# Kernel tuning notes

Measured on AMD Instinct MI355X. Metric: run time of the kernel, lower is better.

Reference implementation:

```python
import jax, jax.numpy as jnp
import numpy as np

H = 128        # hidden_dim
R = 50         # num_rbf
L = 4          # num_layers
CUTOFF = 5.0
N = 10000      # atoms
M = 64         # molecules
BOX = 54.7     # box side -> ~32 neighbors within cutoff
EPS = 1e-5     # LayerNorm eps (torch default)


def setup_inputs() -> dict:
    rng = np.random.default_rng(0)
    positions = rng.uniform(0.0, BOX, size=(N, 3)).astype(np.float32)
    # static radius graph (the torch module filters a dense NxN pair list by cutoff;
    # we do that once here so runtime shapes are fixed / jit-friendly)
    sq = (positions ** 2).sum(-1)
    d2 = sq[:, None] + sq[None, :] - 2.0 * positions @ positions.T
    mask = (d2 < CUTOFF * CUTOFF) & ~np.eye(N, dtype=bool)
    row, col = np.nonzero(mask)
    edge_index = jnp.asarray(np.stack([row, col]).astype(np.int32))  # [2, E]

    key = jax.random.key(0)
    ks = jax.random.split(key, 6)
    s = 0.05
    return dict(
        atomic_numbers=jax.random.randint(ks[0], (N,), 0, 100),
        positions=jnp.asarray(positions),
        batch=jnp.asarray((np.arange(N) * M // N).astype(np.int32)),  # sorted, all M present
        edge_index=edge_index,
        embedding=jax.random.normal(ks[1], (100, H), jnp.float32) * s,
        W1=jax.random.normal(ks[2], (L, H + R, H), jnp.float32) * s,
        b1=jnp.zeros((L, H), jnp.float32),
        W2=jax.random.normal(ks[3], (L, H, H), jnp.float32) * s,
        b2=jnp.zeros((L, H), jnp.float32),
        W_ih=jax.random.normal(ks[4], (L, H, 3 * H), jnp.float32) * s,
        b_ih=jax.random.normal(ks[5], (L, 3 * H), jnp.float32) * s,
        b_hh=jnp.zeros((L, 3 * H), jnp.float32),
        ln_g=jnp.ones((H,), jnp.float32),
        ln_b=jnp.zeros((H,), jnp.float32),
    )


def reference(atomic_numbers, positions, batch, edge_index, embedding,
              W1, b1, W2, b2, W_ih, b_ih, b_hh, ln_g, ln_b):
    x = embedding[jnp.clip(atomic_numbers, 0, 99)]                  # [N, H]
    row, col = edge_index[0], edge_index[1]
    d = jnp.linalg.norm(positions[row] - positions[col], axis=-1)   # [E]
    centers = jnp.linspace(0.0, CUTOFF, R)
    width = CUTOFF / R
    rbf = jnp.exp(-((d[:, None] - centers) ** 2) / (2.0 * width * width))  # [E, R]
    n_atoms = x.shape[0]
    for l in range(L):
        x_j = x[row]                                                # gather [E, H]
        inp = jnp.concatenate([x_j, rbf], axis=-1)                  # [E, H+R]
        msg = jax.nn.silu(inp @ W1[l] + b1[l]) @ W2[l] + b2[l]      # [E, H]
        aggr = jax.ops.segment_sum(msg, col, num_segments=n_atoms)  # [N, H]
        # GRU step with h0 = 0: W_hh @ h vanishes, only b_hh survives
        gi = aggr @ W_ih[l] + b_ih[l]                               # [N, 3H]
        gi_r, gi_z, gi_n = jnp.split(gi, 3, axis=-1)
        bh_r, bh_z, bh_n = jnp.split(b_hh[l], 3)
        r = jax.nn.sigmoid(gi_r + bh_r)
        z = jax.nn.sigmoid(gi_z + bh_z)
        n = jnp.tanh(gi_n + r * bh_n)
        x = x + (1.0 - z) * n                                       # h' = (1-z)*n + z*0
    mu = x.mean(-1, keepdims=True)
    var = ((x - mu) ** 2).mean(-1, keepdims=True)
    x = (x - mu) / jnp.sqrt(var + EPS) * ln_g + ln_b
    sums = jax.ops.segment_sum(x, batch, num_segments=M)            # [M, H]
    counts = jax.ops.segment_sum(jnp.ones((x.shape[0],), jnp.float32), batch, num_segments=M)
    graph_rep = sums / jnp.clip(counts, 1.0)[:, None]
    return x, graph_rep
```

## Files before the change

kernel.cpp:

```cpp
#include <hip/hip_runtime.h>
#include <hip/hip_bf16.h>
#include <math.h>


#define HH 128
#define RR 50
#define LL 4
#define L2E 1.4426950408889634f

typedef __attribute__((ext_vector_type(8))) short short8;
typedef __attribute__((ext_vector_type(4))) float floatx4;

__device__ __forceinline__ unsigned short f2bf(float f) {
    unsigned u = __float_as_uint(f);
    unsigned r = (u + 0x7fffu + ((u >> 16) & 1u)) >> 16;
    return (unsigned short)r;
}
__device__ __forceinline__ unsigned pack_bf2(float lo, float hi) {
    unsigned u0 = __float_as_uint(lo) + 0x8000u;
    unsigned u1 = __float_as_uint(hi) + 0x8000u;
    return __builtin_amdgcn_perm(u1, u0, 0x07060302);
}
__device__ __forceinline__ float fast_sigmoid(float x) {
    return __builtin_amdgcn_rcpf(1.f + __builtin_amdgcn_exp2f(x * (-L2E)));
}
__device__ __forceinline__ float fast_tanh(float x) {
    x = fminf(fmaxf(x, -15.f), 15.f);
    float t = __builtin_amdgcn_exp2f(x * (2.f * L2E));
    return (t - 1.f) * __builtin_amdgcn_rcpf(t + 1.f);
}
__device__ __forceinline__ int imin(int a, int b) { return a < b ? a : b; }

__global__ __launch_bounds__(256) void prep_kernel(
    const int* __restrict__ an, const float* __restrict__ emb,
    float* __restrict__ X,
    const float* __restrict__ pos, const int* __restrict__ erow,
    const int* __restrict__ ecol, float* __restrict__ dist,
    int* __restrict__ rowptr, int* __restrict__ bptr,
    const int* __restrict__ batch,
    const float* __restrict__ W1, unsigned short* __restrict__ W1rT,
    unsigned short* __restrict__ W1xT,
    const float* __restrict__ W2, const float* __restrict__ Wih,
    unsigned short* __restrict__ WcT,
    const float* __restrict__ b2, float* __restrict__ P,
    int N, int E, int M)
{
    int gidx = blockIdx.x * 256 + threadIdx.x;
    int c0 = N * HH;
    if (gidx < c0) {
        int i = gidx >> 7, n = gidx & 127;
        int z = an[i];
        z = z < 0 ? 0 : (z > 99 ? 99 : z);
        X[gidx] = emb[z * HH + n];
        return;
    }
    gidx -= c0;
    int PT = E > N ? E : N;
    if (gidx < PT) {
        int i = gidx;
        if (i < E) {
            int rc = erow[i];
            int rp = (i > 0) ? erow[i - 1] : -1;
            for (int r = rp + 1; r <= rc; ++r) rowptr[r] = i;
            if (i == E - 1)
                for (int r = rc + 1; r <= N; ++r) rowptr[r] = E;
        }
        if (i < N) {
            int bc = batch[i];
            int bp = (i > 0) ? batch[i - 1] : -1;
            for (int m = bp + 1; m <= bc; ++m) bptr[m] = i;
            if (i == N - 1)
                for (int m = bc + 1; m <= M; ++m) bptr[m] = N;
        }
        return;
    }
    gidx -= PT;
    if (gidx < E) {
        int e = gidx;
        int r = erow[e], c = ecol[e];
        float dx = pos[r * 3 + 0] - pos[c * 3 + 0];
        float dy = pos[r * 3 + 1] - pos[c * 3 + 1];
        float dz = pos[r * 3 + 2] - pos[c * 3 + 2];
        dist[e] = sqrtf(dx * dx + dy * dy + dz * dz);
        return;
    }
    gidx -= E;
    if (gidx < LL * HH * 64) {
        int l = gidx >> 13, rem = gidx & 8191;
        int f = rem >> 9, lane2 = (rem >> 3) & 63, j = rem & 7;
        int nt = f >> 1, h = f & 1;
        int n = nt * 16 + (lane2 & 15);
        int k = h * 32 + (lane2 >> 4) * 8 + j;
        float v = (k < RR) ? W1[((size_t)l * 178 + 128 + k) * HH + n] : 0.f;
        W1rT[gidx] = f2bf(v);
        return;
    }
    gidx -= LL * HH * 64;
    if (gidx < LL * HH * HH) {
        int l = gidx >> 14, rem = gidx & 16383, n = rem >> 7, k = rem & 127;
        W1xT[gidx] = f2bf(W1[((size_t)l * 178 + k) * HH + n]);
        return;
    }
    gidx -= LL * HH * HH;
    if (gidx < LL * HH * 384) {
        int l = gidx / (HH * 384), rem = gidx % (HH * 384);
        int i = rem / 384, j = rem % 384;
        const float* w2row = W2 + ((size_t)l * HH + i) * HH;
        const float* wih = Wih + (size_t)l * HH * 384;
        float acc = 0.f;
#pragma unroll 4
        for (int k = 0; k < HH; ++k)
            acc = fmaf(w2row[k], wih[(size_t)k * 384 + j], acc);
        WcT[((size_t)l * 384 + j) * HH + i] = f2bf(acc);
        return;
    }
    gidx -= LL * HH * 384;
    if (gidx < LL * 384) {
        int l = gidx / 384, j = gidx % 384;
        const float* b2l = b2 + (size_t)l * HH;
        const float* wih = Wih + (size_t)l * HH * 384;
        float acc = 0.f;
#pragma unroll 4
        for (int k = 0; k < HH; ++k)
            acc = fmaf(b2l[k], wih[(size_t)k * 384 + j], acc);
        P[gidx] = acc;
    }
}

#define XAB 32
__global__ __launch_bounds__(256) void xw_kernel(
    const float* __restrict__ X, const float* __restrict__ W,
    const float* __restrict__ bias, unsigned short* __restrict__ XWb, int N)
{
    __shared__ __align__(16) float A[XAB][HH];
    int tid = threadIdx.x;
    int abase = blockIdx.x * XAB;
    for (int idx = tid; idx < XAB * HH; idx += 256) {
        int a = idx >> 7, k = idx & 127;
        A[a][k] = (abase + a < N) ? X[(size_t)(abase + a) * HH + k] : 0.f;
    }
    __syncthreads();
    int n = tid & 127, s = tid >> 7;
    float acc[16];
#pragma unroll
    for (int i = 0; i < 16; ++i) acc[i] = 0.f;
    for (int kc = 0; kc < 32; ++kc) {
        float w0 = W[(4 * kc + 0) * HH + n];
        float w1 = W[(4 * kc + 1) * HH + n];
        float w2 = W[(4 * kc + 2) * HH + n];
        float w3 = W[(4 * kc + 3) * HH + n];
#pragma unroll
        for (int i = 0; i < 16; ++i) {
            float4 av = *(const float4*)&A[s * 16 + i][4 * kc];
            acc[i] = fmaf(av.x, w0, acc[i]);
            acc[i] = fmaf(av.y, w1, acc[i]);
            acc[i] = fmaf(av.z, w2, acc[i]);
            acc[i] = fmaf(av.w, w3, acc[i]);
        }
    }
    float b = bias[n];
#pragma unroll
    for (int i = 0; i < 16; ++i) {
        int a = abase + s * 16 + i;
        if (a < N) XWb[(size_t)a * HH + n] = f2bf(acc[i] + b);
    }
}

__global__ __launch_bounds__(256) void edge_mfma_kernel(
    const unsigned short* __restrict__ XWb, const unsigned short* __restrict__ W1rTf,
    const float* __restrict__ dist, const int* __restrict__ rowptr,
    const int* __restrict__ ecol, unsigned short* __restrict__ Sbf,
    int N, int nwaves)
{
    __shared__ __align__(16) unsigned short W1s[8192];
    int tid = threadIdx.x;
    {
        const uint4* src = (const uint4*)W1rTf;
        uint4* dst = (uint4*)W1s;
#pragma unroll
        for (int i = 0; i < 4; ++i) dst[tid + i * 256] = src[tid + i * 256];
    }
    __syncthreads();

    int wid = (blockIdx.x << 2) + (tid >> 6);
    int lane = tid & 63;
    int c = lane & 15, q = lane >> 4;

    const float stepc = 5.0f / 49.0f;
    const float negc = -50.f * L2E;
    float kqs = (float)(q << 3) * stepc;

    int NW = 2 * N;
    for (int w = wid; w < NW; w += nwaves) {
        int a = w >> 1, h = w & 1;
        int es = rowptr[a], ee = rowptr[a + 1];
        float acc[4][4];
#pragma unroll
        for (int t = 0; t < 4; ++t)
#pragma unroll
            for (int r = 0; r < 4; ++r) acc[t][r] = 0.f;

        if (es < ee) {
            int last = ee - 1;
            int ce0 = imin(es + c, last);
            float dcur = dist[ce0];
            int colcur = ecol[ce0];
            int ce1 = imin(es + 16 + c, last);
            float dnxt = dist[ce1];
            int colnxt = ecol[ce1];

            for (int eb = es; eb < ee; eb += 16) {
                const unsigned short* xwrow = XWb + (size_t)colcur * HH + h * 64;
                uint2 gx[4];
#pragma unroll
                for (int t = 0; t < 4; ++t)
                    gx[t] = *(const uint2*)&xwrow[t * 16 + (q << 2)];

                float d_t = dcur;
                dcur = dnxt; colcur = colnxt;
                int ce2 = imin(eb + 32 + c, last);
                dnxt = dist[ce2];
                colnxt = ecol[ce2];

                float dq0 = d_t - kqs;
                float dq1 = dq0 - 32.f * stepc;
                union { unsigned u[4]; short8 s; } ub0, ub1;
#pragma unroll
                for (int p = 0; p < 4; ++p) {
                    float t0 = dq0 - (float)(2 * p) * stepc;
                    float t1 = dq0 - (float)(2 * p + 1) * stepc;
                    float e0f = __builtin_amdgcn_exp2f(negc * t0 * t0);
                    float e1f = __builtin_amdgcn_exp2f(negc * t1 * t1);
                    ub0.u[p] = pack_bf2(e0f, e1f);
                    float t2 = dq1 - (float)(2 * p) * stepc;
                    float t3 = dq1 - (float)(2 * p + 1) * stepc;
                    float e2f = __builtin_amdgcn_exp2f(negc * t2 * t2);
                    float e3f = __builtin_amdgcn_exp2f(negc * t3 * t3);
                    ub1.u[p] = pack_bf2(e2f, e3f);
                }
                short8 B0 = ub0.s, B1 = ub1.s;
                float msk = ((eb + c) < ee) ? 1.f : 0.f;

                unsigned wbyte = (unsigned)(lane * 16);
                asm volatile("" : "+v"(wbyte));
                const char* Wlp = (const char*)W1s + wbyte;

#pragma unroll
                for (int t = 0; t < 4; ++t) {
                    int f0 = (h * 4 + t) * 2;
                    short8 A0 = *(const short8*)(Wlp + f0 * 1024);
                    short8 A1 = *(const short8*)(Wlp + (f0 + 1) * 1024);
                    floatx4 C;
                    C[0] = __uint_as_float(gx[t].x << 16);
                    C[1] = __uint_as_float(gx[t].x & 0xffff0000u);
                    C[2] = __uint_as_float(gx[t].y << 16);
                    C[3] = __uint_as_float(gx[t].y & 0xffff0000u);
                    C = __builtin_amdgcn_mfma_f32_16x16x32_bf16(A0, B0, C, 0, 0, 0);
                    C = __builtin_amdgcn_mfma_f32_16x16x32_bf16(A1, B1, C, 0, 0, 0);
#pragma unroll
                    for (int r = 0; r < 4; ++r) {
                        float hh = C[r];
                        float v = hh * fast_sigmoid(hh);
                        acc[t][r] = fmaf(v, msk, acc[t][r]);
                    }
                }
            }
        }

        int b0 = c & 1, b1 = (c >> 1) & 1, b2 = (c >> 2) & 1, b3 = (c >> 3) & 1;
        float s1[4][2];
#pragma unroll
        for (int t = 0; t < 4; ++t)
#pragma unroll
            for (int p = 0; p < 2; ++p) {
                float keep = b0 ? acc[t][2 * p + 1] : acc[t][2 * p];
                float send = b0 ? acc[t][2 * p] : acc[t][2 * p + 1];
                s1[t][p] = keep + __shfl_xor(send, 1, 64);
            }
        float s2[4];
#pragma unroll
        for (int t = 0; t < 4; ++t) {
            float keep = b1 ? s1[t][1] : s1[t][0];
            float send = b1 ? s1[t][0] : s1[t][1];
            s2[t] = keep + __shfl_xor(send, 2, 64);
        }
        float s3[2];
#pragma unroll
        for (int u = 0; u < 2; ++u) {
            float keep = b2 ? s2[2 * u + 1] : s2[2 * u];
            float send = b2 ? s2[2 * u] : s2[2 * u + 1];
            s3[u] = keep + __shfl_xor(send, 4, 64);
        }
        float keep = b3 ? s3[1] : s3[0];
        float send = b3 ? s3[0] : s3[1];
        float fin = keep + __shfl_xor(send, 8, 64);

        int t_fin = 2 * b3 + b2;
        int r_fin = 2 * b1 + b0;
        int n = t_fin * 16 + (q << 2) + r_fin;
        Sbf[(size_t)a * HH + h * 64 + n] = f2bf(fin);
    }
}

#define GA 32
__global__ __launch_bounds__(256) void grux_mfma_kernel(
    const unsigned short* __restrict__ Sbf, const unsigned short* __restrict__ WcT,
    const float* __restrict__ P, const float* __restrict__ bih,
    const float* __restrict__ bhh, const int* __restrict__ rowptr,
    float* __restrict__ X, int N,
    const unsigned short* __restrict__ W1xT, const float* __restrict__ b1next,
    unsigned short* __restrict__ XWb, int do_xw)
{
    __shared__ __align__(16) unsigned short Sb[GA][136];
    __shared__ __align__(16) unsigned short Xb[GA][136];
    int tid = threadIdx.x;
    int abase = blockIdx.x * GA;
    int w = tid >> 6, lane = tid & 63, c = lane & 15, q = lane >> 4;

    float pn[2][3], bi[2][3], bh[2][3], deg[2][4];
#pragma unroll
    for (int t = 0; t < 2; ++t) {
        int n = w * 32 + t * 16 + c;
#pragma unroll
        for (int g = 0; g < 3; ++g) {
            pn[t][g] = P[g * 128 + n];
            bi[t][g] = bih[g * 128 + n];
            bh[t][g] = bhh[g * 128 + n];
        }
    }
#pragma unroll
    for (int sub = 0; sub < 2; ++sub)
#pragma unroll
        for (int r = 0; r < 4; ++r) {
            int a = abase + sub * 16 + q * 4 + r;
            deg[sub][r] = (a < N) ? (float)(rowptr[a + 1] - rowptr[a]) : 0.f;
        }

    {
        int a = tid >> 3, ch = tid & 7;
        int aa = abase + a; if (aa >= N) aa = N - 1;
        const uint4* src = (const uint4*)(Sbf + (size_t)aa * HH + ch * 16);
        uint4 v0 = src[0];
        uint4 v1 = src[1];
        uint4* dst = (uint4*)&Sb[a][ch * 16];
        dst[0] = v0;
        dst[1] = v1;
    }
    __syncthreads();

    floatx4 Cg[3][2][2];
#pragma unroll
    for (int g = 0; g < 3; ++g)
#pragma unroll
        for (int t = 0; t < 2; ++t)
#pragma unroll
            for (int sub = 0; sub < 2; ++sub)
                Cg[g][t][sub] = floatx4{0.f, 0.f, 0.f, 0.f};

#pragma unroll
    for (int kt = 0; kt < 4; ++kt) {
        short8 A0 = *(const short8*)&Sb[c][kt * 32 + q * 8];
        short8 A1 = *(const short8*)&Sb[16 + c][kt * 32 + q * 8];
#pragma unroll
        for (int g = 0; g < 3; ++g)
#pragma unroll
            for (int t = 0; t < 2; ++t) {
                int nrow = g * 128 + w * 32 + t * 16 + c;
                short8 B = *(const short8*)&WcT[(size_t)nrow * HH + kt * 32 + q * 8];
                Cg[g][t][0] = __builtin_amdgcn_mfma_f32_16x16x32_bf16(A0, B, Cg[g][t][0], 0, 0, 0);
                Cg[g][t][1] = __builtin_amdgcn_mfma_f32_16x16x32_bf16(A1, B, Cg[g][t][1], 0, 0, 0);
            }
    }

#pragma unroll
    for (int sub = 0; sub < 2; ++sub)
#pragma unroll
        for (int r = 0; r < 4; ++r) {
            int am = sub * 16 + q * 4 + r;
            int a = abase + am;
            bool ok = a < N;
#pragma unroll
            for (int t = 0; t < 2; ++t) {
                int n = w * 32 + t * 16 + c;
                float g0 = Cg[0][t][sub][r] + deg[sub][r] * pn[t][0] + bi[t][0];
                float g1 = Cg[1][t][sub][r] + deg[sub][r] * pn[t][1] + bi[t][1];
                float g2 = Cg[2][t][sub][r] + deg[sub][r] * pn[t][2] + bi[t][2];
                float rr = fast_sigmoid(g0 + bh[t][0]);
                float zz = fast_sigmoid(g1 + bh[t][1]);
                float nn = fast_tanh(g2 + rr * bh[t][2]);
                float xv = 0.f;
                if (ok) {
                    xv = X[(size_t)a * HH + n] + (1.f - zz) * nn;
                    X[(size_t)a * HH + n] = xv;
                }
                Xb[am][n] = f2bf(xv);
            }
        }

    if (!do_xw) return;
    __syncthreads();

    floatx4 Cx[2][2];
#pragma unroll
    for (int t = 0; t < 2; ++t)
#pragma unroll
        for (int sub = 0; sub < 2; ++sub)
            Cx[t][sub] = floatx4{0.f, 0.f, 0.f, 0.f};
#pragma unroll
    for (int kt = 0; kt < 4; ++kt) {
        short8 A0 = *(const short8*)&Xb[c][kt * 32 + q * 8];
        short8 A1 = *(const short8*)&Xb[16 + c][kt * 32 + q * 8];
#pragma unroll
        for (int t = 0; t < 2; ++t) {
            int nrow = w * 32 + t * 16 + c;
            short8 B = *(const short8*)&W1xT[(size_t)nrow * HH + kt * 32 + q * 8];
            Cx[t][0] = __builtin_amdgcn_mfma_f32_16x16x32_bf16(A0, B, Cx[t][0], 0, 0, 0);
            Cx[t][1] = __builtin_amdgcn_mfma_f32_16x16x32_bf16(A1, B, Cx[t][1], 0, 0, 0);
        }
    }
#pragma unroll
    for (int sub = 0; sub < 2; ++sub)
#pragma unroll
        for (int r = 0; r < 4; ++r) {
            int a = abase + sub * 16 + q * 4 + r;
            if (a >= N) continue;
#pragma unroll
            for (int t = 0; t < 2; ++t) {
                int n = w * 32 + t * 16 + c;
                XWb[(size_t)a * HH + n] = f2bf(Cx[t][sub][r] + b1next[n]);
            }
        }
}

__global__ __launch_bounds__(1024) void lnpool_kernel(
    const float* __restrict__ X, const float* __restrict__ g,
    const float* __restrict__ b, const int* __restrict__ bptr,
    float* __restrict__ outx, float* __restrict__ outg, int N)
{
    __shared__ float sm[16][128];
    int m = blockIdx.x, tid = threadIdx.x;
    int wv = tid >> 6, lane = tid & 63;
    int a0 = bptr[m], a1 = bptr[m + 1];
    float g0 = g[lane], g1 = g[64 + lane];
    float bb0 = b[lane], bb1 = b[64 + lane];
    float acc0 = 0.f, acc1 = 0.f;
    for (int a = a0 + wv; a < a1; a += 16) {
        float v0 = X[(size_t)a * HH + lane];
        float v1 = X[(size_t)a * HH + 64 + lane];
        float smv = v0 + v1;
        for (int off = 32; off > 0; off >>= 1) smv += __shfl_xor(smv, off, 64);
        float mu = smv * (1.f / 128.f);
        float d0 = v0 - mu, d1 = v1 - mu;
        float vq = d0 * d0 + d1 * d1;
        for (int off = 32; off > 0; off >>= 1) vq += __shfl_xor(vq, off, 64);
        float inv = rsqrtf(vq * (1.f / 128.f) + 1e-5f);
        float y0 = d0 * inv * g0 + bb0;
        float y1 = d1 * inv * g1 + bb1;
        outx[(size_t)a * HH + lane] = y0;
        outx[(size_t)a * HH + 64 + lane] = y1;
        acc0 += y0;
        acc1 += y1;
    }
    sm[wv][lane] = acc0;
    sm[wv][64 + lane] = acc1;
    __syncthreads();
    if (tid < 128) {
        float s = 0.f;
#pragma unroll
        for (int i = 0; i < 16; ++i) s += sm[i][tid];
        float cnt = (float)(a1 - a0);
        outg[(size_t)m * HH + tid] = s / fmaxf(cnt, 1.f);
    }
}

extern "C" void kernel_launch(void* const* d_in, const int* in_sizes, int n_in,
                              void* d_out, int out_size, void* d_ws, size_t ws_size,
                              hipStream_t stream)
{
    const int*   an   = (const int*)d_in[0];
    const float* pos  = (const float*)d_in[1];
    const int*   bat  = (const int*)d_in[2];
    const int*   eidx = (const int*)d_in[3];
    const float* emb  = (const float*)d_in[4];
    const float* W1   = (const float*)d_in[5];
    const float* b1   = (const float*)d_in[6];
    const float* W2   = (const float*)d_in[7];
    const float* b2   = (const float*)d_in[8];
    const float* Wih  = (const float*)d_in[9];
    const float* bih  = (const float*)d_in[10];
    const float* bhh  = (const float*)d_in[11];
    const float* lng  = (const float*)d_in[12];
    const float* lnb  = (const float*)d_in[13];

    int N = in_sizes[0];
    int E = in_sizes[3] / 2;
    int M = out_size / HH - N;
    const int* erow = eidx;
    const int* ecol = eidx + E;

    float* ws   = (float*)d_ws;
    size_t off = 0;
    float* X    = ws + off; off += (size_t)N * HH;
    unsigned short* Sbf = (unsigned short*)(ws + off); off += (size_t)N * HH / 2;
    unsigned short* XWb = (unsigned short*)(ws + off); off += (size_t)N * HH / 2;
    float* P    = ws + off; off += LL * 384;
    float* dist = ws + off; off += E;
    int* rowptr = (int*)(ws + off); off += N + 1;
    int* bptr   = (int*)(ws + off); off += M + 1;
    off = (off + 3) & ~(size_t)3;
    unsigned short* W1rT = (unsigned short*)(ws + off); off += (size_t)LL * HH * 32;
    unsigned short* W1xT = (unsigned short*)(ws + off); off += (size_t)LL * HH * 64;
    unsigned short* WcT  = (unsigned short*)(ws + off); off += (size_t)LL * 384 * 64;

    float* outx = (float*)d_out;
    float* outg = outx + (size_t)N * HH;

    int PT = (E > N ? E : N);
    long total = (long)N * HH + PT + E + LL * HH * 64 + LL * HH * HH
               + LL * HH * 384 + LL * 384;
    int prep_blocks = (int)((total + 255) / 256);

    prep_kernel<<<prep_blocks, 256, 0, stream>>>(
        an, emb, X, pos, erow, ecol, dist, rowptr, bptr, bat,
        W1, W1rT, W1xT, W2, Wih, WcT, b2, P, N, E, M);

    xw_kernel<<<(N + XAB - 1) / XAB, 256, 0, stream>>>(X, W1, b1, XWb, N);

    int eblocks = (2 * N + 3) / 4;
    int nwaves = eblocks * 4;
    int grux_blocks = (N + GA - 1) / GA;
    for (int l = 0; l < LL; ++l) {
        edge_mfma_kernel<<<eblocks, 256, 0, stream>>>(
            XWb, W1rT + (size_t)l * HH * 64, dist, rowptr, ecol, Sbf, N, nwaves);
        int do_xw = (l < LL - 1) ? 1 : 0;
        int ln = (l + 1 < LL) ? l + 1 : l;
        grux_mfma_kernel<<<grux_blocks, 256, 0, stream>>>(
            Sbf, WcT + (size_t)l * 384 * HH, P + l * 384,
            bih + l * 384, bhh + l * 384, rowptr, X, N,
            W1xT + (size_t)ln * HH * HH, b1 + (size_t)ln * HH, XWb, do_xw);
    }

    lnpool_kernel<<<M, 1024, 0, stream>>>(X, lng, lnb, bptr, outx, outg, N);
}
```

Baseline: 317.2 us.

## Fold first-layer XW into embedding table and fuse LayerNorm pooling into last GRU

Precomputes embedding@W1+b1 for all 100 atom types in the prep kernel, so the first edge layer gathers rows through the clipped atomic number and the separate xw_kernel launch goes away. The final GRU kernel now applies LayerNorm in shared memory and accumulates per-molecule means with shared and global atomics, which removes the lnpool kernel and the last write and reread of X. The cost is an extra dependent index load per edge in layer 0, atomic float sums that make the pooled output order-dependent, and the assumption that each block of GA atoms spans at most two molecules.

```diff
diff --git a/kernel.cpp b/kernel.cpp
--- a/kernel.cpp
+++ b/kernel.cpp
@@ -43,6 +43,8 @@
     const float* __restrict__ W2, const float* __restrict__ Wih,
     unsigned short* __restrict__ WcT,
     const float* __restrict__ b2, float* __restrict__ P,
+    const float* __restrict__ b1, unsigned short* __restrict__ embWbf,
+    int* __restrict__ zc, float* __restrict__ outg,
     int N, int E, int M)
 {
     int gidx = blockIdx.x * 256 + threadIdx.x;
@@ -124,53 +126,36 @@
         for (int k = 0; k < HH; ++k)
             acc = fmaf(b2l[k], wih[(size_t)k * 384 + j], acc);
         P[gidx] = acc;
-    }
-}
-
-#define XAB 32
-__global__ __launch_bounds__(256) void xw_kernel(
-    const float* __restrict__ X, const float* __restrict__ W,
-    const float* __restrict__ bias, unsigned short* __restrict__ XWb, int N)
-{
-    __shared__ __align__(16) float A[XAB][HH];
-    int tid = threadIdx.x;
-    int abase = blockIdx.x * XAB;
-    for (int idx = tid; idx < XAB * HH; idx += 256) {
-        int a = idx >> 7, k = idx & 127;
-        A[a][k] = (abase + a < N) ? X[(size_t)(abase + a) * HH + k] : 0.f;
-    }
-    __syncthreads();
-    int n = tid & 127, s = tid >> 7;
-    float acc[16];
-#pragma unroll
-    for (int i = 0; i < 16; ++i) acc[i] = 0.f;
-    for (int kc = 0; kc < 32; ++kc) {
-        float w0 = W[(4 * kc + 0) * HH + n];
-        float w1 = W[(4 * kc + 1) * HH + n];
-        float w2 = W[(4 * kc + 2) * HH + n];
-        float w3 = W[(4 * kc + 3) * HH + n];
-#pragma unroll
-        for (int i = 0; i < 16; ++i) {
-            float4 av = *(const float4*)&A[s * 16 + i][4 * kc];
-            acc[i] = fmaf(av.x, w0, acc[i]);
-            acc[i] = fmaf(av.y, w1, acc[i]);
-            acc[i] = fmaf(av.z, w2, acc[i]);
-            acc[i] = fmaf(av.w, w3, acc[i]);
-        }
-    }
-    float b = bias[n];
-#pragma unroll
-    for (int i = 0; i < 16; ++i) {
-        int a = abase + s * 16 + i;
-        if (a < N) XWb[(size_t)a * HH + n] = f2bf(acc[i] + b);
+        return;
+    }
+    gidx -= LL * 384;
+    if (gidx < N) {
+        int z = an[gidx];
+        zc[gidx] = z < 0 ? 0 : (z > 99 ? 99 : z);
+        return;
+    }
+    gidx -= N;
+    if (gidx < 100 * HH) {
+        int z = gidx >> 7, n = gidx & 127;
+        const float* er = emb + (size_t)z * HH;
+        float acc = b1[n];
+#pragma unroll 4
+        for (int k = 0; k < HH; ++k)
+            acc = fmaf(er[k], W1[(size_t)k * HH + n], acc);
+        embWbf[gidx] = f2bf(acc);
+        return;
+    }
+    gidx -= 100 * HH;
+    if (gidx < M * HH) {
+        outg[gidx] = 0.f;
     }
 }
 
 __global__ __launch_bounds__(256) void edge_mfma_kernel(
-    const unsigned short* __restrict__ XWb, const unsigned short* __restrict__ W1rTf,
+    const unsigned short* __restrict__ Xsrc, const unsigned short* __restrict__ W1rTf,
     const float* __restrict__ dist, const int* __restrict__ rowptr,
-    const int* __restrict__ ecol, unsigned short* __restrict__ Sbf,
-    int N, int nwaves)
+    const int* __restrict__ ecol, const int* __restrict__ zc, int use_z,
+    unsigned short* __restrict__ Sbf, int N, int nwaves)
 {
     __shared__ __align__(16) unsigned short W1s[8192];
     int tid = threadIdx.x;
@@ -204,23 +189,26 @@
             int last = ee - 1;
             int ce0 = imin(es + c, last);
             float dcur = dist[ce0];
-            int colcur = ecol[ce0];
+            int c0raw = ecol[ce0];
+            int rowcur = use_z ? zc[c0raw] : c0raw;
             int ce1 = imin(es + 16 + c, last);
             float dnxt = dist[ce1];
             int colnxt = ecol[ce1];
 
             for (int eb = es; eb < ee; eb += 16) {
-                const unsigned short* xwrow = XWb + (size_t)colcur * HH + h * 64;
+                const unsigned short* xwrow = Xsrc + (size_t)rowcur * HH + h * 64;
                 uint2 gx[4];
 #pragma unroll
                 for (int t = 0; t < 4; ++t)
                     gx[t] = *(const uint2*)&xwrow[t * 16 + (q << 2)];
 
                 float d_t = dcur;
-                dcur = dnxt; colcur = colnxt;
+                dcur = dnxt;
+                int rownxt = use_z ? zc[colnxt] : colnxt;
                 int ce2 = imin(eb + 32 + c, last);
                 dnxt = dist[ce2];
                 colnxt = ecol[ce2];
+                rowcur = rownxt;
 
                 float dq0 = d_t - kqs;
                 float dq1 = dq0 - 32.f * stepc;
@@ -309,10 +297,20 @@
     const float* __restrict__ bhh, const int* __restrict__ rowptr,
     float* __restrict__ X, int N,
     const unsigned short* __restrict__ W1xT, const float* __restrict__ b1next,
-    unsigned short* __restrict__ XWb, int do_xw)
+    unsigned short* __restrict__ XWb, int do_xw,
+    int do_ln, const float* __restrict__ lng, const float* __restrict__ lnb,
+    const int* __restrict__ batch, const int* __restrict__ bptr,
+    float* __restrict__ outx, float* __restrict__ outg)
 {
-    __shared__ __align__(16) unsigned short Sb[GA][136];
-    __shared__ __align__(16) unsigned short Xb[GA][136];
+    __shared__ __align__(16) union ShMem {
+        struct { unsigned short Sb[GA][136]; unsigned short Xb[GA][136]; } s;
+        struct { float Xf[GA][132]; float pool[2][HH]; } f;
+    } u;
+    unsigned short (&Sb)[GA][136] = u.s.Sb;
+    unsigned short (&Xb)[GA][136] = u.s.Xb;
+    float (&Xf)[GA][132] = u.f.Xf;
+    float (&pool)[2][HH] = u.f.pool;
+
     int tid = threadIdx.x;
     int abase = blockIdx.x * GA;
     int w = tid >> 6, lane = tid & 63, c = lane & 15, q = lane >> 4;
@@ -371,6 +369,8 @@
                 Cg[g][t][1] = __builtin_amdgcn_mfma_f32_16x16x32_bf16(A1, B, Cg[g][t][1], 0, 0, 0);
             }
     }
+
+    if (do_ln) __syncthreads();
 
 #pragma unroll
     for (int sub = 0; sub < 2; ++sub)
@@ -391,11 +391,75 @@
                 float xv = 0.f;
                 if (ok) {
                     xv = X[(size_t)a * HH + n] + (1.f - zz) * nn;
-                    X[(size_t)a * HH + n] = xv;
+                    if (!do_ln) X[(size_t)a * HH + n] = xv;
                 }
-                Xb[am][n] = f2bf(xv);
+                if (do_ln) Xf[am][n] = xv;
+                else       Xb[am][n] = f2bf(xv);
             }
         }
+
+    if (do_ln) {
+        (&pool[0][0])[tid] = 0.f;
+        __syncthreads();
+
+        int row = tid >> 3, j = tid & 7;
+        int a2 = abase + row;
+        float4 x0 = *(const float4*)&Xf[row][j * 16];
+        float4 x1 = *(const float4*)&Xf[row][j * 16 + 4];
+        float4 x2 = *(const float4*)&Xf[row][j * 16 + 8];
+        float4 x3 = *(const float4*)&Xf[row][j * 16 + 12];
+        float s = x0.x + x0.y + x0.z + x0.w + x1.x + x1.y + x1.z + x1.w
+                + x2.x + x2.y + x2.z + x2.w + x3.x + x3.y + x3.z + x3.w;
+        s += __shfl_xor(s, 1, 64);
+        s += __shfl_xor(s, 2, 64);
+        s += __shfl_xor(s, 4, 64);
+        float mu = s * (1.f / 128.f);
+        float qv = 0.f;
+#define QACC(v) { float dx=(v).x-mu, dy=(v).y-mu, dz=(v).z-mu, dw=(v).w-mu; \
+                  qv += dx*dx + dy*dy + dz*dz + dw*dw; }
+        QACC(x0) QACC(x1) QACC(x2) QACC(x3)
+#undef QACC
+        qv += __shfl_xor(qv, 1, 64);
+        qv += __shfl_xor(qv, 2, 64);
+        qv += __shfl_xor(qv, 4, 64);
+        float inv = rsqrtf(qv * (1.f / 128.f) + 1e-5f);
+
+        int m0 = batch[abase];
+        if (a2 < N) {
+            int midx = batch[a2] - m0;
+            const float4* gg = (const float4*)&lng[j * 16];
+            const float4* bb = (const float4*)&lnb[j * 16];
+            float* outrow = outx + (size_t)a2 * HH + j * 16;
+            float* pl = &pool[midx][j * 16];
+            float4 xs[4] = {x0, x1, x2, x3};
+#pragma unroll
+            for (int i = 0; i < 4; ++i) {
+                float4 gv = gg[i], bv = bb[i], xv4 = xs[i];
+                float4 y;
+                y.x = (xv4.x - mu) * inv * gv.x + bv.x;
+                y.y = (xv4.y - mu) * inv * gv.y + bv.y;
+                y.z = (xv4.z - mu) * inv * gv.z + bv.z;
+                y.w = (xv4.w - mu) * inv * gv.w + bv.w;
+                *(float4*)(outrow + i * 4) = y;
+                atomicAdd(pl + i * 4 + 0, y.x);
+                atomicAdd(pl + i * 4 + 1, y.y);
+                atomicAdd(pl + i * 4 + 2, y.z);
+                atomicAdd(pl + i * 4 + 3, y.w);
+            }
+        }
+        __syncthreads();
+
+        int a_last = abase + GA - 1; if (a_last >= N) a_last = N - 1;
+        int mlast = batch[a_last];
+        int mi = tid >> 7, col = tid & 127;
+        int m = m0 + mi;
+        if (m <= mlast) {
+            float cnt = (float)(bptr[m + 1] - bptr[m]);
+            float invc = 1.f / fmaxf(cnt, 1.f);
+            atomicAdd(&outg[(size_t)m * HH + col], pool[mi][col] * invc);
+        }
+        return;
+    }
 
     if (!do_xw) return;
     __syncthreads();
@@ -430,47 +494,6 @@
                 XWb[(size_t)a * HH + n] = f2bf(Cx[t][sub][r] + b1next[n]);
             }
         }
-}
-
-__global__ __launch_bounds__(1024) void lnpool_kernel(
-    const float* __restrict__ X, const float* __restrict__ g,
-    const float* __restrict__ b, const int* __restrict__ bptr,
-    float* __restrict__ outx, float* __restrict__ outg, int N)
-{
-    __shared__ float sm[16][128];
-    int m = blockIdx.x, tid = threadIdx.x;
-    int wv = tid >> 6, lane = tid & 63;
-    int a0 = bptr[m], a1 = bptr[m + 1];
-    float g0 = g[lane], g1 = g[64 + lane];
-    float bb0 = b[lane], bb1 = b[64 + lane];
-    float acc0 = 0.f, acc1 = 0.f;
-    for (int a = a0 + wv; a < a1; a += 16) {
-        float v0 = X[(size_t)a * HH + lane];
-        float v1 = X[(size_t)a * HH + 64 + lane];
-        float smv = v0 + v1;
-        for (int off = 32; off > 0; off >>= 1) smv += __shfl_xor(smv, off, 64);
-        float mu = smv * (1.f / 128.f);
-        float d0 = v0 - mu, d1 = v1 - mu;
-        float vq = d0 * d0 + d1 * d1;
-        for (int off = 32; off > 0; off >>= 1) vq += __shfl_xor(vq, off, 64);
-        float inv = rsqrtf(vq * (1.f / 128.f) + 1e-5f);
-        float y0 = d0 * inv * g0 + bb0;
-        float y1 = d1 * inv * g1 + bb1;
-        outx[(size_t)a * HH + lane] = y0;
-        outx[(size_t)a * HH + 64 + lane] = y1;
-        acc0 += y0;
-        acc1 += y1;
-    }
-    sm[wv][lane] = acc0;
-    sm[wv][64 + lane] = acc1;
-    __syncthreads();
-    if (tid < 128) {
-        float s = 0.f;
-#pragma unroll
-        for (int i = 0; i < 16; ++i) s += sm[i][tid];
-        float cnt = (float)(a1 - a0);
-        outg[(size_t)m * HH + tid] = s / fmaxf(cnt, 1.f);
-    }
 }
 
 extern "C" void kernel_launch(void* const* d_in, const int* in_sizes, int n_in,
@@ -511,34 +534,36 @@
     unsigned short* W1rT = (unsigned short*)(ws + off); off += (size_t)LL * HH * 32;
     unsigned short* W1xT = (unsigned short*)(ws + off); off += (size_t)LL * HH * 64;
     unsigned short* WcT  = (unsigned short*)(ws + off); off += (size_t)LL * 384 * 64;
+    unsigned short* embWbf = (unsigned short*)(ws + off); off += (size_t)100 * HH / 2;
+    int* zc     = (int*)(ws + off); off += N;
 
     float* outx = (float*)d_out;
     float* outg = outx + (size_t)N * HH;
 
     int PT = (E > N ? E : N);
     long total = (long)N * HH + PT + E + LL * HH * 64 + LL * HH * HH
-               + LL * HH * 384 + LL * 384;
+               + LL * HH * 384 + LL * 384 + N + 100 * HH + (long)M * HH;
     int prep_blocks = (int)((total + 255) / 256);
 
     prep_kernel<<<prep_blocks, 256, 0, stream>>>(
         an, emb, X, pos, erow, ecol, dist, rowptr, bptr, bat,
-        W1, W1rT, W1xT, W2, Wih, WcT, b2, P, N, E, M);
-
-    xw_kernel<<<(N + XAB - 1) / XAB, 256, 0, stream>>>(X, W1, b1, XWb, N);
+        W1, W1rT, W1xT, W2, Wih, WcT, b2, P,
+        b1, embWbf, zc, outg, N, E, M);
 
     int eblocks = (2 * N + 3) / 4;
     int nwaves = eblocks * 4;
     int grux_blocks = (N + GA - 1) / GA;
     for (int l = 0; l < LL; ++l) {
         edge_mfma_kernel<<<eblocks, 256, 0, stream>>>(
-            XWb, W1rT + (size_t)l * HH * 64, dist, rowptr, ecol, Sbf, N, nwaves);
+            (l == 0) ? embWbf : XWb, W1rT + (size_t)l * HH * 64,
+            dist, rowptr, ecol, zc, (l == 0) ? 1 : 0, Sbf, N, nwaves);
         int do_xw = (l < LL - 1) ? 1 : 0;
+        int do_ln = (l == LL - 1) ? 1 : 0;
         int ln = (l + 1 < LL) ? l + 1 : l;
         grux_mfma_kernel<<<grux_blocks, 256, 0, stream>>>(
             Sbf, WcT + (size_t)l * 384 * HH, P + l * 384,
             bih + l * 384, bhh + l * 384, rowptr, X, N,
-            W1xT + (size_t)ln * HH * HH, b1 + (size_t)ln * HH, XWb, do_xw);
-    }
-
-    lnpool_kernel<<<M, 1024, 0, stream>>>(X, lng, lnb, bptr, outx, outg, N);
-}
+            W1xT + (size_t)ln * HH * HH, b1 + (size_t)ln * HH, XWb, do_xw,
+            do_ln, lng, lnb, bat, bptr, outx, outg);
+    }
+}
```

Result: faster. 305.5 us (-3.7%).
